# Performance work log

Hardware: AMD Instinct MI355X
Metric: run time of the kernel (lower is better)

Reference implementation:

```python
import jax, jax.numpy as jnp
import numpy as np

BN_EPS = 1e-3  # O-CNN default bn_eps


def setup_inputs() -> dict:
    key = jax.random.key(0)
    k1, k2, k3 = jax.random.split(key, 3)
    N, Cin, Cout, K = 100000, 32, 32, 27  # nodes, channels, 3x3x3 taps
    data_in = jax.random.normal(k1, (1, Cin, N, 1), dtype=jnp.float32)
    neigh = jax.random.randint(k2, (N, K), 0, N, dtype=jnp.int32)
    weight = jax.random.normal(k3, (K, Cin, Cout), dtype=jnp.float32) * 0.05
    gamma = jnp.ones((Cout,), dtype=jnp.float32)
    beta = jnp.zeros((Cout,), dtype=jnp.float32)
    return {"data_in": data_in, "neigh": neigh, "weight": weight,
            "gamma": gamma, "beta": beta}


def reference(data_in, neigh, weight, gamma, beta):
    # data_in: [1, Cin, N, 1] -> x: [N, Cin]
    x = data_in[0, :, :, 0].T
    # Octree conv: gather 27 neighbor features per node, then small matmul.
    col = x[neigh]                                   # [N, 27, Cin] (irregular gather)
    y = jnp.einsum('nkc,kcd->nd', col, weight)       # [N, Cout]
    # BatchNorm2d in training mode: stats over the N (spatial) axis.
    mean = jnp.mean(y, axis=0)
    var = jnp.mean(jnp.square(y - mean), axis=0)     # biased variance, as BN uses
    yn = (y - mean) * jax.lax.rsqrt(var + BN_EPS) * gamma + beta
    # back to O-CNN layout [1, Cout, N, 1]
    return yn.T[None, :, :, None]
```

## Files before the change

### kernel.cpp

```cpp
#include <hip/hip_runtime.h>

#define KK 27

typedef short bf16x8 __attribute__((ext_vector_type(8)));
typedef float f32x4  __attribute__((ext_vector_type(4)));

__device__ inline unsigned short f2bf(float f) {
    unsigned u = __float_as_uint(f);
    unsigned r = u + 0x7fffu + ((u >> 16) & 1u);
    return (unsigned short)(r >> 16);
}

__global__ __launch_bounds__(256) void prep_k(const float* __restrict__ in,
                                              const float* __restrict__ w,
                                              unsigned short* __restrict__ xTb,
                                              unsigned short* __restrict__ wTb,
                                              int N, int nxblk) {
    __shared__ float tile[32][33];
    const int b = blockIdx.x;
    if (b < nxblk) {
        int n0 = b * 32;
        int tx = threadIdx.x & 31;
        int ty = threadIdx.x >> 5;
#pragma unroll
        for (int c = ty; c < 32; c += 8) {
            int n = n0 + tx;
            tile[c][tx] = (n < N) ? in[(long)c * N + n] : 0.f;
        }
        __syncthreads();
#pragma unroll
        for (int nn = ty; nn < 32; nn += 8) {
            int n = n0 + nn;
            if (n < N) xTb[(long)n * 32 + tx] = f2bf(tile[tx][nn]);
        }
        if (b == 0 && threadIdx.x < 32) xTb[(long)N * 32 + threadIdx.x] = 0;
    } else {
        int k = b - nxblk;
        for (int i = threadIdx.x; i < 1024; i += 256) {
            int cin = i >> 5, cout = i & 31;
            wTb[k * 1024 + cout * 32 + cin] = f2bf(w[k * 1024 + cin * 32 + cout]);
        }
    }
}

template <int CNT>
__device__ __forceinline__ void conv_taps(int k0,
                                          const unsigned short* __restrict__ xTb,
                                          const int* __restrict__ neigh,
                                          const unsigned short* __restrict__ wTb,
                                          long nb0, long nb1, bool v0, bool v1,
                                          int r16, int quad, int N,
                                          f32x4& acc00, f32x4& acc01,
                                          f32x4& acc10, f32x4& acc11) {
    bf16x8 A0[3], A1[3], B0[3], B1[3];
    int ja[3], jb[3];

#pragma unroll
    for (int d = 0; d < 3; ++d) {
        int kk = k0 + (d < CNT ? d : CNT - 1);
        ja[d] = v0 ? neigh[nb0 + kk] : N;
        jb[d] = v1 ? neigh[nb1 + kk] : N;
    }
#pragma unroll
    for (int d = 0; d < 3; ++d) {
        int kk = k0 + (d < CNT ? d : CNT - 1);
        A0[d] = *(const bf16x8*)(xTb + (long)ja[d] * 32 + quad * 8);
        A1[d] = *(const bf16x8*)(xTb + (long)jb[d] * 32 + quad * 8);
        const unsigned short* wn = wTb + kk * 1024;
        B0[d] = *(const bf16x8*)(wn + r16 * 32 + quad * 8);
        B1[d] = *(const bf16x8*)(wn + (16 + r16) * 32 + quad * 8);
        int k2 = k0 + (d + 3 < CNT ? d + 3 : CNT - 1);
        ja[d] = v0 ? neigh[nb0 + k2] : N;
        jb[d] = v1 ? neigh[nb1 + k2] : N;
    }
#pragma unroll
    for (int t = 0; t < CNT; ++t) {
        const int cur = t % 3;
        acc00 = __builtin_amdgcn_mfma_f32_16x16x32_bf16(A0[cur], B0[cur], acc00, 0, 0, 0);
        acc01 = __builtin_amdgcn_mfma_f32_16x16x32_bf16(A0[cur], B1[cur], acc01, 0, 0, 0);
        acc10 = __builtin_amdgcn_mfma_f32_16x16x32_bf16(A1[cur], B0[cur], acc10, 0, 0, 0);
        acc11 = __builtin_amdgcn_mfma_f32_16x16x32_bf16(A1[cur], B1[cur], acc11, 0, 0, 0);
        if (t + 3 < CNT) {
            const int kk = k0 + t + 3;
            A0[cur] = *(const bf16x8*)(xTb + (long)ja[cur] * 32 + quad * 8);
            A1[cur] = *(const bf16x8*)(xTb + (long)jb[cur] * 32 + quad * 8);
            const unsigned short* wn = wTb + kk * 1024;
            B0[cur] = *(const bf16x8*)(wn + r16 * 32 + quad * 8);
            B1[cur] = *(const bf16x8*)(wn + (16 + r16) * 32 + quad * 8);
            const int k2 = k0 + (t + 6 < CNT ? t + 6 : CNT - 1);
            ja[cur] = v0 ? neigh[nb0 + k2] : N;
            jb[cur] = v1 ? neigh[nb1 + k2] : N;
        }
    }
}

__global__ __launch_bounds__(256, 4) void conv_k(const unsigned short* __restrict__ xTb,
                                                 const int* __restrict__ neigh,
                                                 const unsigned short* __restrict__ wTb,
                                                 float* __restrict__ y,
                                                 float* __restrict__ tot,
                                                 int N) {
    __shared__ float cmb[2][16][64];
    __shared__ float ct[2][32][33];
    __shared__ float pr[4][16];

    const int tid   = threadIdx.x;
    const int L     = tid & 63;
    const int w     = tid >> 6;
    const int gi    = w >> 1;
    const int khalf = w & 1;
    const int r16   = L & 15;
    const int quad  = L >> 4;
    const int base  = blockIdx.x * 64 + gi * 32;
    const int n0 = base + r16;
    const int n1 = base + 16 + r16;
    const bool v0 = (n0 < N), v1 = (n1 < N);
    const long nb0 = (long)(v0 ? n0 : 0) * KK;
    const long nb1 = (long)(v1 ? n1 : 0) * KK;

    f32x4 acc00 = {0.f, 0.f, 0.f, 0.f};
    f32x4 acc01 = acc00, acc10 = acc00, acc11 = acc00;

    if (khalf == 0)
        conv_taps<14>(0,  xTb, neigh, wTb, nb0, nb1, v0, v1, r16, quad, N,
                      acc00, acc01, acc10, acc11);
    else
        conv_taps<13>(14, xTb, neigh, wTb, nb0, nb1, v0, v1, r16, quad, N,
                      acc00, acc01, acc10, acc11);

    if (khalf == 1) {
#pragma unroll
        for (int r = 0; r < 4; ++r) {
            cmb[gi][r][L]      = acc00[r];
            cmb[gi][4 + r][L]  = acc01[r];
            cmb[gi][8 + r][L]  = acc10[r];
            cmb[gi][12 + r][L] = acc11[r];
        }
    }
    __syncthreads();

    float s0 = 0.f, q0 = 0.f, s1 = 0.f, q1 = 0.f;
    if (khalf == 0) {
#pragma unroll
        for (int r = 0; r < 4; ++r) {
            acc00[r] += cmb[gi][r][L];
            acc01[r] += cmb[gi][4 + r][L];
            acc10[r] += cmb[gi][8 + r][L];
            acc11[r] += cmb[gi][12 + r][L];
        }

#pragma unroll
        for (int r = 0; r < 4; ++r) {
            s0 += acc00[r] + acc10[r];
            q0 += acc00[r] * acc00[r] + acc10[r] * acc10[r];
            s1 += acc01[r] + acc11[r];
            q1 += acc01[r] * acc01[r] + acc11[r] * acc11[r];
        }
#pragma unroll
        for (int off = 16; off < 64; off <<= 1) {
            s0 += __shfl_xor(s0, off, 64);
            q0 += __shfl_xor(q0, off, 64);
            s1 += __shfl_xor(s1, off, 64);
            q1 += __shfl_xor(q1, off, 64);
        }
        if (w == 2 && L < 16) {
            pr[0][L] = s0; pr[1][L] = s1; pr[2][L] = q0; pr[3][L] = q1;
        }

#pragma unroll
        for (int r = 0; r < 4; ++r) {
            ct[gi][quad * 4 + r][r16]           = acc00[r];
            ct[gi][quad * 4 + r][16 + r16]      = acc01[r];
            ct[gi][16 + quad * 4 + r][r16]      = acc10[r];
            ct[gi][16 + quad * 4 + r][16 + r16] = acc11[r];
        }
    }
    __syncthreads();

    if (w == 0 && L < 16) {
        atomicAdd(&tot[L],      s0 + pr[0][L]);
        atomicAdd(&tot[L + 16], s1 + pr[1][L]);
        atomicAdd(&tot[L + 32], q0 + pr[2][L]);
        atomicAdd(&tot[L + 48], q1 + pr[3][L]);
    }

    const int node = tid & 63;
    const int gn = blockIdx.x * 64 + node;
    if (gn < N) {
#pragma unroll
        for (int i = 0; i < 8; ++i) {
            const int cout = (tid >> 6) * 8 + i;
            y[(long)cout * N + gn] = ct[node >> 5][node & 31][cout];
        }
    }
}

__global__ __launch_bounds__(256) void norm_k(float* __restrict__ y,
                                              const float* __restrict__ tot,
                                              const float* __restrict__ gamma,
                                              const float* __restrict__ beta, int N) {
    const int d = blockIdx.y;
    const float mean = tot[d] / (float)N;
    const float var  = tot[d + 32] / (float)N - mean * mean;
    const float sc   = gamma[d] * rsqrtf(var + 1e-3f);
    const float sh   = beta[d] - mean * sc;

    int i = blockIdx.x * blockDim.x + threadIdx.x;
    int base = i * 4;
    if (base + 3 < N) {
        float4* p = (float4*)(y + (long)d * N + base);
        float4 v = *p;
        v.x = fmaf(v.x, sc, sh);
        v.y = fmaf(v.y, sc, sh);
        v.z = fmaf(v.z, sc, sh);
        v.w = fmaf(v.w, sc, sh);
        *p = v;
    } else if (base < N) {
        for (int t = base; t < N; ++t) y[(long)d * N + t] = fmaf(y[(long)d * N + t], sc, sh);
    }
}

extern "C" void kernel_launch(void* const* d_in, const int* in_sizes, int n_in,
                              void* d_out, int out_size, void* d_ws, size_t ws_size,
                              hipStream_t stream) {
    const float* data_in = (const float*)d_in[0];
    const int*   neigh   = (const int*)d_in[1];
    const float* weight  = (const float*)d_in[2];
    const float* gamma   = (const float*)d_in[3];
    const float* beta    = (const float*)d_in[4];
    float* out = (float*)d_out;

    const int N = in_sizes[1] / KK;
    const int nxblk  = (N + 31) / 32;
    const int nblk64 = (N + 63) / 64;

    char* ws = (char*)d_ws;
    unsigned short* xTb = (unsigned short*)ws;
    unsigned short* wTb = (unsigned short*)(ws + (size_t)(N + 1) * 64);
    float* tot = (float*)(ws + (size_t)(N + 1) * 64 + 55296);

    hipMemsetAsync(tot, 0, 64 * sizeof(float), stream);
    prep_k<<<nxblk + KK, 256, 0, stream>>>(data_in, weight, xTb, wTb, N, nxblk);
    conv_k<<<nblk64, 256, 0, stream>>>(xTb, neigh, wTb, out, tot, N);
    dim3 ngrid(((N + 3) / 4 + 255) / 256, 32);
    norm_k<<<ngrid, 256, 0, stream>>>(out, tot, gamma, beta, N);
}
```

Before: 151.9 us.

## Use one-wave conv blocks per 16 nodes with striped BN stat atomics

Rewrites the conv kernel so each 64-thread block covers 16 nodes and runs all 27 taps in one wave. This removes the K-split across waves, its shared-memory combine and the extra barrier. BN statistics are accumulated into 32 striped partial buffers to reduce atomic contention, and norm_k sums the stripes. The tot zeroing moves from a memset into prep_k, which drops one API call. The cost is many more small blocks, a serial 27-tap MFMA chain per wave, and uncoalesced 16-wide output stores.

Measured after the change: 135.6 us. -10.8%, faster.

```diff
diff --git a/kernel.cpp b/kernel.cpp
--- a/kernel.cpp
+++ b/kernel.cpp
@@ -15,6 +15,7 @@
                                               const float* __restrict__ w,
                                               unsigned short* __restrict__ xTb,
                                               unsigned short* __restrict__ wTb,
+                                              float* __restrict__ tot,
                                               int N, int nxblk) {
     __shared__ float tile[32][33];
     const int b = blockIdx.x;
@@ -40,157 +41,97 @@
             int cin = i >> 5, cout = i & 31;
             wTb[k * 1024 + cout * 32 + cin] = f2bf(w[k * 1024 + cin * 32 + cout]);
         }
-    }
-}
-
-template <int CNT>
-__device__ __forceinline__ void conv_taps(int k0,
-                                          const unsigned short* __restrict__ xTb,
-                                          const int* __restrict__ neigh,
-                                          const unsigned short* __restrict__ wTb,
-                                          long nb0, long nb1, bool v0, bool v1,
-                                          int r16, int quad, int N,
-                                          f32x4& acc00, f32x4& acc01,
-                                          f32x4& acc10, f32x4& acc11) {
-    bf16x8 A0[3], A1[3], B0[3], B1[3];
-    int ja[3], jb[3];
-
-#pragma unroll
-    for (int d = 0; d < 3; ++d) {
-        int kk = k0 + (d < CNT ? d : CNT - 1);
-        ja[d] = v0 ? neigh[nb0 + kk] : N;
-        jb[d] = v1 ? neigh[nb1 + kk] : N;
-    }
-#pragma unroll
-    for (int d = 0; d < 3; ++d) {
-        int kk = k0 + (d < CNT ? d : CNT - 1);
-        A0[d] = *(const bf16x8*)(xTb + (long)ja[d] * 32 + quad * 8);
-        A1[d] = *(const bf16x8*)(xTb + (long)jb[d] * 32 + quad * 8);
-        const unsigned short* wn = wTb + kk * 1024;
-        B0[d] = *(const bf16x8*)(wn + r16 * 32 + quad * 8);
-        B1[d] = *(const bf16x8*)(wn + (16 + r16) * 32 + quad * 8);
-        int k2 = k0 + (d + 3 < CNT ? d + 3 : CNT - 1);
-        ja[d] = v0 ? neigh[nb0 + k2] : N;
-        jb[d] = v1 ? neigh[nb1 + k2] : N;
-    }
-#pragma unroll
-    for (int t = 0; t < CNT; ++t) {
-        const int cur = t % 3;
-        acc00 = __builtin_amdgcn_mfma_f32_16x16x32_bf16(A0[cur], B0[cur], acc00, 0, 0, 0);
-        acc01 = __builtin_amdgcn_mfma_f32_16x16x32_bf16(A0[cur], B1[cur], acc01, 0, 0, 0);
-        acc10 = __builtin_amdgcn_mfma_f32_16x16x32_bf16(A1[cur], B0[cur], acc10, 0, 0, 0);
-        acc11 = __builtin_amdgcn_mfma_f32_16x16x32_bf16(A1[cur], B1[cur], acc11, 0, 0, 0);
-        if (t + 3 < CNT) {
-            const int kk = k0 + t + 3;
-            A0[cur] = *(const bf16x8*)(xTb + (long)ja[cur] * 32 + quad * 8);
-            A1[cur] = *(const bf16x8*)(xTb + (long)jb[cur] * 32 + quad * 8);
-            const unsigned short* wn = wTb + kk * 1024;
-            B0[cur] = *(const bf16x8*)(wn + r16 * 32 + quad * 8);
-            B1[cur] = *(const bf16x8*)(wn + (16 + r16) * 32 + quad * 8);
-            const int k2 = k0 + (t + 6 < CNT ? t + 6 : CNT - 1);
-            ja[cur] = v0 ? neigh[nb0 + k2] : N;
-            jb[cur] = v1 ? neigh[nb1 + k2] : N;
+        if (k == 0) {
+            for (int i = threadIdx.x; i < 32 * 64; i += 256) tot[i] = 0.f;
         }
     }
 }
 
-__global__ __launch_bounds__(256, 4) void conv_k(const unsigned short* __restrict__ xTb,
-                                                 const int* __restrict__ neigh,
-                                                 const unsigned short* __restrict__ wTb,
-                                                 float* __restrict__ y,
-                                                 float* __restrict__ tot,
-                                                 int N) {
-    __shared__ float cmb[2][16][64];
-    __shared__ float ct[2][32][33];
-    __shared__ float pr[4][16];
+__global__ __launch_bounds__(64, 4) void conv_k(const unsigned short* __restrict__ xTb,
+                                                const int* __restrict__ neigh,
+                                                const unsigned short* __restrict__ wTb,
+                                                float* __restrict__ y,
+                                                float* __restrict__ tot,
+                                                int N) {
+    __shared__ float ct[16][33];
 
-    const int tid   = threadIdx.x;
-    const int L     = tid & 63;
-    const int w     = tid >> 6;
-    const int gi    = w >> 1;
-    const int khalf = w & 1;
-    const int r16   = L & 15;
-    const int quad  = L >> 4;
-    const int base  = blockIdx.x * 64 + gi * 32;
-    const int n0 = base + r16;
-    const int n1 = base + 16 + r16;
-    const bool v0 = (n0 < N), v1 = (n1 < N);
+    const int L    = threadIdx.x;
+    const int r16  = L & 15;
+    const int quad = L >> 4;
+    const int base = blockIdx.x * 16;
+    const int n0   = base + r16;
+    const bool v0  = (n0 < N);
     const long nb0 = (long)(v0 ? n0 : 0) * KK;
-    const long nb1 = (long)(v1 ? n1 : 0) * KK;
 
-    f32x4 acc00 = {0.f, 0.f, 0.f, 0.f};
-    f32x4 acc01 = acc00, acc10 = acc00, acc11 = acc00;
+    f32x4 acc0 = {0.f, 0.f, 0.f, 0.f};
+    f32x4 acc1 = acc0;
 
-    if (khalf == 0)
-        conv_taps<14>(0,  xTb, neigh, wTb, nb0, nb1, v0, v1, r16, quad, N,
-                      acc00, acc01, acc10, acc11);
-    else
-        conv_taps<13>(14, xTb, neigh, wTb, nb0, nb1, v0, v1, r16, quad, N,
-                      acc00, acc01, acc10, acc11);
+    bf16x8 A[3], B0[3], B1[3];
+    int ja[3];
 
-    if (khalf == 1) {
 #pragma unroll
-        for (int r = 0; r < 4; ++r) {
-            cmb[gi][r][L]      = acc00[r];
-            cmb[gi][4 + r][L]  = acc01[r];
-            cmb[gi][8 + r][L]  = acc10[r];
-            cmb[gi][12 + r][L] = acc11[r];
+    for (int d = 0; d < 3; ++d) ja[d] = v0 ? neigh[nb0 + d] : N;
+#pragma unroll
+    for (int d = 0; d < 3; ++d) {
+        A[d]  = *(const bf16x8*)(xTb + (long)ja[d] * 32 + quad * 8);
+        const unsigned short* wn = wTb + d * 1024;
+        B0[d] = *(const bf16x8*)(wn + r16 * 32 + quad * 8);
+        B1[d] = *(const bf16x8*)(wn + (16 + r16) * 32 + quad * 8);
+        ja[d] = v0 ? neigh[nb0 + d + 3] : N;
+    }
+
+#pragma unroll
+    for (int t = 0; t < KK; ++t) {
+        const int cur = t % 3;
+        acc0 = __builtin_amdgcn_mfma_f32_16x16x32_bf16(A[cur], B0[cur], acc0, 0, 0, 0);
+        acc1 = __builtin_amdgcn_mfma_f32_16x16x32_bf16(A[cur], B1[cur], acc1, 0, 0, 0);
+        if (t + 3 < KK) {
+            A[cur]  = *(const bf16x8*)(xTb + (long)ja[cur] * 32 + quad * 8);
+            const unsigned short* wn = wTb + (t + 3) * 1024;
+            B0[cur] = *(const bf16x8*)(wn + r16 * 32 + quad * 8);
+            B1[cur] = *(const bf16x8*)(wn + (16 + r16) * 32 + quad * 8);
+            if (t + 6 < KK) ja[cur] = v0 ? neigh[nb0 + t + 6] : N;
         }
     }
-    __syncthreads();
 
     float s0 = 0.f, q0 = 0.f, s1 = 0.f, q1 = 0.f;
-    if (khalf == 0) {
 #pragma unroll
-        for (int r = 0; r < 4; ++r) {
-            acc00[r] += cmb[gi][r][L];
-            acc01[r] += cmb[gi][4 + r][L];
-            acc10[r] += cmb[gi][8 + r][L];
-            acc11[r] += cmb[gi][12 + r][L];
-        }
+    for (int r = 0; r < 4; ++r) {
+        s0 += acc0[r];
+        q0 += acc0[r] * acc0[r];
+        s1 += acc1[r];
+        q1 += acc1[r] * acc1[r];
+    }
+#pragma unroll
+    for (int off = 16; off < 64; off <<= 1) {
+        s0 += __shfl_xor(s0, off, 64);
+        q0 += __shfl_xor(q0, off, 64);
+        s1 += __shfl_xor(s1, off, 64);
+        q1 += __shfl_xor(q1, off, 64);
+    }
+    const int stripe = blockIdx.x & 31;
+    if (L < 16) {
+        float* tb = tot + stripe * 64;
+        atomicAdd(&tb[L],      s0);
+        atomicAdd(&tb[L + 16], s1);
+        atomicAdd(&tb[L + 32], q0);
+        atomicAdd(&tb[L + 48], q1);
+    }
 
 #pragma unroll
-        for (int r = 0; r < 4; ++r) {
-            s0 += acc00[r] + acc10[r];
-            q0 += acc00[r] * acc00[r] + acc10[r] * acc10[r];
-            s1 += acc01[r] + acc11[r];
-            q1 += acc01[r] * acc01[r] + acc11[r] * acc11[r];
-        }
-#pragma unroll
-        for (int off = 16; off < 64; off <<= 1) {
-            s0 += __shfl_xor(s0, off, 64);
-            q0 += __shfl_xor(q0, off, 64);
-            s1 += __shfl_xor(s1, off, 64);
-            q1 += __shfl_xor(q1, off, 64);
-        }
-        if (w == 2 && L < 16) {
-            pr[0][L] = s0; pr[1][L] = s1; pr[2][L] = q0; pr[3][L] = q1;
-        }
-
-#pragma unroll
-        for (int r = 0; r < 4; ++r) {
-            ct[gi][quad * 4 + r][r16]           = acc00[r];
-            ct[gi][quad * 4 + r][16 + r16]      = acc01[r];
-            ct[gi][16 + quad * 4 + r][r16]      = acc10[r];
-            ct[gi][16 + quad * 4 + r][16 + r16] = acc11[r];
-        }
+    for (int r = 0; r < 4; ++r) {
+        ct[quad * 4 + r][r16]      = acc0[r];
+        ct[quad * 4 + r][16 + r16] = acc1[r];
     }
     __syncthreads();
-
-    if (w == 0 && L < 16) {
-        atomicAdd(&tot[L],      s0 + pr[0][L]);
-        atomicAdd(&tot[L + 16], s1 + pr[1][L]);
-        atomicAdd(&tot[L + 32], q0 + pr[2][L]);
-        atomicAdd(&tot[L + 48], q1 + pr[3][L]);
-    }
-
-    const int node = tid & 63;
-    const int gn = blockIdx.x * 64 + node;
+    const int node = L & 15;
+    const int ch   = L >> 4;
+    const int gn   = base + node;
     if (gn < N) {
 #pragma unroll
         for (int i = 0; i < 8; ++i) {
-            const int cout = (tid >> 6) * 8 + i;
-            y[(long)cout * N + gn] = ct[node >> 5][node & 31][cout];
+            const int cout = ch * 8 + i;
+            y[(long)cout * N + gn] = ct[node][cout];
         }
     }
 }
@@ -200,8 +141,14 @@
                                               const float* __restrict__ gamma,
                                               const float* __restrict__ beta, int N) {
     const int d = blockIdx.y;
-    const float mean = tot[d] / (float)N;
-    const float var  = tot[d + 32] / (float)N - mean * mean;
+    float sm = 0.f, sq = 0.f;
+#pragma unroll
+    for (int s = 0; s < 32; ++s) {
+        sm += tot[s * 64 + d];
+        sq += tot[s * 64 + 32 + d];
+    }
+    const float mean = sm / (float)N;
+    const float var  = sq / (float)N - mean * mean;
     const float sc   = gamma[d] * rsqrtf(var + 1e-3f);
     const float sh   = beta[d] - mean * sc;
 
@@ -232,16 +179,15 @@
 
     const int N = in_sizes[1] / KK;
     const int nxblk  = (N + 31) / 32;
-    const int nblk64 = (N + 63) / 64;
+    const int nblk16 = (N + 15) / 16;
 
     char* ws = (char*)d_ws;
     unsigned short* xTb = (unsigned short*)ws;
     unsigned short* wTb = (unsigned short*)(ws + (size_t)(N + 1) * 64);
     float* tot = (float*)(ws + (size_t)(N + 1) * 64 + 55296);
 
-    hipMemsetAsync(tot, 0, 64 * sizeof(float), stream);
-    prep_k<<<nxblk + KK, 256, 0, stream>>>(data_in, weight, xTb, wTb, N, nxblk);
-    conv_k<<<nblk64, 256, 0, stream>>>(xTb, neigh, wTb, out, tot, N);
+    prep_k<<<nxblk + KK, 256, 0, stream>>>(data_in, weight, xTb, wTb, tot, N, nxblk);
+    conv_k<<<nblk16, 64, 0, stream>>>(xTb, neigh, wTb, out, tot, N);
     dim3 ngrid(((N + 3) / 4 + 255) / 256, 32);
     norm_k<<<ngrid, 256, 0, stream>>>(out, tot, gamma, beta, N);
 }
```
